# Kernel tuning notes

Measured on AMD Instinct MI355X. Metric: run time of the kernel, lower is better.

The kernel has to match this reference:

```python
import jax, jax.numpy as jnp
import numpy as np

B, C, D = 8192, 1000, 2048
CLAMP_MIN, CLAMP_MAX = 1e-12, 1e12
SEP_WEIGHT = 0.001


def setup_inputs() -> dict:
    key = jax.random.key(0)
    k1, k2, k3 = jax.random.split(key, 3)
    x = jax.random.normal(k1, (B, D), dtype=jnp.float32)
    centers = jax.random.normal(k2, (C, D), dtype=jnp.float32)
    labels = jax.random.randint(k3, (B,), 0, C, dtype=jnp.int64)
    return {"x": x, "centers": centers, "labels": labels}


def reference(x, centers, labels):
    distmat = (
        jnp.sum(x * x, axis=1, keepdims=True)
        + jnp.sum(centers * centers, axis=1)[None, :]
        - 2.0 * (x @ centers.T)
    )
    d = jnp.clip(distmat, CLAMP_MIN, CLAMP_MAX)
    mask = labels[:, None] == jnp.arange(C, dtype=labels.dtype)[None, :]  # [B, C]
    bsz = x.shape[0]
    ncls = centers.shape[0]
    # each row has exactly one True in mask -> counts are B and B*(C-1)
    center_loss = jnp.sum(jnp.where(mask, d, 0.0)) / bsz
    sep_loss = jnp.sum(jnp.where(mask, 0.0, d)) / (bsz * (ncls - 1))
    return center_loss - SEP_WEIGHT * sep_loss
```

## Files before the change

### kernel.cpp

```cpp
#include <hip/hip_runtime.h>


#define DD 2048
#define NB 8192
#define NC 1000
#define D4 (DD / 4)
#define HALF4 256
#define THREADS 256
#define XROWS 8
#define XBLOCKS ((NB / XROWS) * 2)
#define CTILES 8
#define CRG 8
#define CBLOCKS (CTILES * CRG)

#define CQ_OFF   0
#define SC_OFF   65536
#define CSQ_OFF  73728
#define PART_OFF 73984

__device__ __forceinline__ float dot4(float4 a, float4 b) {
    return a.x * b.x + a.y * b.y + a.z * b.z + a.w * b.w;
}
__device__ __forceinline__ void acc4(float4& a, float4 b) {
    a.x += b.x; a.y += b.y; a.z += b.z; a.w += b.w;
}

__global__ __launch_bounds__(THREADS) void centers_kernel(
        const float4* __restrict__ c4, float4* __restrict__ cq,
        float* __restrict__ csq_part) {
    const int t = threadIdx.x;
    const int tile = blockIdx.x & (CTILES - 1);
    const int rg = blockIdx.x >> 3;
    const int col4 = tile * 64 + (t & 63);
    const int rlane = t >> 6;
    const int row0 = rg * 125;

    float4 acc = make_float4(0.f, 0.f, 0.f, 0.f);
    float csq = 0.f;
#pragma unroll 4
    for (int r = rlane; r < 125; r += 4) {
        float4 v = c4[(size_t)(row0 + r) * D4 + col4];
        acc4(acc, v);
        csq += dot4(v, v);
    }

    __shared__ float4 lds[4][64];
    lds[rlane][t & 63] = acc;
    __syncthreads();
    if (t < 64) {
        float4 s = lds[0][t];
        acc4(s, lds[1][t]); acc4(s, lds[2][t]); acc4(s, lds[3][t]);
        cq[rg * 512 + tile * 64 + t] = s;
    }

    __shared__ float red[THREADS / 64];
    for (int off = 32; off > 0; off >>= 1) csq += __shfl_down(csq, off, 64);
    const int lane = t & 63, wv = t >> 6;
    if (lane == 0) red[wv] = csq;
    __syncthreads();
    if (t == 0)
        csq_part[blockIdx.x] = red[0] + red[1] + red[2] + red[3];
}

__global__ __launch_bounds__(THREADS) void sc_fold_kernel(
        const float4* __restrict__ cq, float4* __restrict__ sc4) {
    const int idx = blockIdx.x * THREADS + threadIdx.x;
    float4 s = cq[idx];
#pragma unroll
    for (int r = 1; r < CRG; ++r) acc4(s, cq[r * 512 + idx]);
    sc4[idx] = s;
}

__global__ __launch_bounds__(THREADS) void x_kernel(
        const float4* __restrict__ x4, const float4* __restrict__ c4,
        const int* __restrict__ labels, const float4* __restrict__ sc4,
        float4* __restrict__ partials) {
    const int t = threadIdx.x;
    const int b = blockIdx.x;
    const int rowgrp = b >> 1;
    const int h = (b & 1) * HALF4;
    const int rows0 = rowgrp * XROWS;

    const float4* xr = x4 + (size_t)rows0 * D4 + h + t;
    const float4* cbase = c4 + h + t;

    float4 xa = xr[0];
    float4 xb = xr[D4];

    const int4* l4 = (const int4*)(labels + rows0);
    const int4 la = l4[0], lb = l4[1];
    const int labs[XROWS] = {la.x, la.y, la.z, la.w, lb.x, lb.y, lb.z, lb.w};

    const float4 sc = sc4[h + t];

    float4 ca = cbase[(size_t)labs[0] * D4];
    float4 cb = cbase[(size_t)labs[1] * D4];

    float sx = 0.f, sdot = 0.f, scl = 0.f, s2 = 0.f;

#pragma unroll
    for (int r = 0; r < XROWS; ++r) {
        float4 nx, nc;
        if (r + 2 < XROWS) {
            nx = xr[(size_t)(r + 2) * D4];
            nc = cbase[(size_t)labs[r + 2] * D4];
        }
        sx   += dot4(xa, xa);
        sdot += dot4(xa, ca);
        scl  += dot4(ca, ca);
        s2   += dot4(xa, sc);
        xa = xb; ca = cb;
        if (r + 2 < XROWS) { xb = nx; cb = nc; }
    }

    __shared__ float red[4][THREADS / 64];
    for (int off = 32; off > 0; off >>= 1) {
        sx   += __shfl_down(sx, off, 64);
        sdot += __shfl_down(sdot, off, 64);
        scl  += __shfl_down(scl, off, 64);
        s2   += __shfl_down(s2, off, 64);
    }
    const int lane = t & 63, wv = t >> 6;
    if (lane == 0) {
        red[0][wv] = sx; red[1][wv] = sdot;
        red[2][wv] = scl; red[3][wv] = s2;
    }
    __syncthreads();
    if (t == 0) {
        float4 s;
        s.x = red[0][0] + red[0][1] + red[0][2] + red[0][3];
        s.y = red[1][0] + red[1][1] + red[1][2] + red[1][3];
        s.z = red[2][0] + red[2][1] + red[2][2] + red[2][3];
        s.w = red[3][0] + red[3][1] + red[3][2] + red[3][3];
        partials[b] = s;
    }
}

__global__ __launch_bounds__(THREADS) void finalize_kernel(
        const float4* __restrict__ partials, const float* __restrict__ csq_part,
        float* __restrict__ out) {
    const int t = threadIdx.x;

    double sx = 0.0, sdot = 0.0, scl = 0.0, s2 = 0.0, csq = 0.0;
    for (int i = t; i < XBLOCKS; i += THREADS) {
        float4 p = partials[i];
        sx += (double)p.x; sdot += (double)p.y;
        scl += (double)p.z; s2 += (double)p.w;
    }
    if (t < CBLOCKS) csq = (double)csq_part[t];

    __shared__ double red[5][THREADS / 64];
    for (int off = 32; off > 0; off >>= 1) {
        sx   += __shfl_down(sx, off, 64);
        sdot += __shfl_down(sdot, off, 64);
        scl  += __shfl_down(scl, off, 64);
        s2   += __shfl_down(s2, off, 64);
        csq  += __shfl_down(csq, off, 64);
    }
    const int lane = t & 63, wv = t >> 6;
    if (lane == 0) {
        red[0][wv] = sx; red[1][wv] = sdot; red[2][wv] = scl;
        red[3][wv] = s2; red[4][wv] = csq;
    }
    __syncthreads();
    if (t == 0) {
        double Sx   = red[0][0] + red[0][1] + red[0][2] + red[0][3];
        double Sdot = red[1][0] + red[1][1] + red[1][2] + red[1][3];
        double Scl  = red[2][0] + red[2][1] + red[2][2] + red[2][3];
        double S2   = red[3][0] + red[3][1] + red[3][2] + red[3][3];
        double Sc   = red[4][0] + red[4][1] + red[4][2] + red[4][3];
        double sum_all  = (double)NC * Sx + (double)NB * Sc - 2.0 * S2;
        double sum_diag = Sx + Scl - 2.0 * Sdot;
        double center_loss = sum_diag / (double)NB;
        double sep_loss =
            (sum_all - sum_diag) / ((double)NB * (double)(NC - 1));
        out[0] = (float)(center_loss - 0.001 * sep_loss);
    }
}

extern "C" void kernel_launch(void* const* d_in, const int* in_sizes, int n_in,
                              void* d_out, int out_size, void* d_ws, size_t ws_size,
                              hipStream_t stream) {
    const float4* x4 = (const float4*)d_in[0];
    const float4* c4 = (const float4*)d_in[1];
    const int* labels = (const int*)d_in[2];

    float4* cq = (float4*)((char*)d_ws + CQ_OFF);
    float4* sc = (float4*)((char*)d_ws + SC_OFF);
    float* csq_part = (float*)((char*)d_ws + CSQ_OFF);
    float4* partials = (float4*)((char*)d_ws + PART_OFF);
    float* out = (float*)d_out;

    centers_kernel<<<CBLOCKS, THREADS, 0, stream>>>(c4, cq, csq_part);
    sc_fold_kernel<<<2, THREADS, 0, stream>>>((const float4*)cq, sc);
    x_kernel<<<XBLOCKS, THREADS, 0, stream>>>(x4, c4, labels,
                                              (const float4*)sc, partials);
    finalize_kernel<<<1, THREADS, 0, stream>>>(partials, csq_part, out);
}
```

Baseline: 110.7 us.

## Counting-sort rows by label so center gathers hit cache

An extra block in the centers kernel builds a label histogram, prefix-scans it, and writes a permutation of row indices grouped by label along with the sorted labels. The x kernel then processes rows in that order, so consecutive rows share the same center row and the gathered center reads should reuse cache instead of scattering. The cost is a serial single-block sort on the critical path before x_kernel, plus x rows now read non-contiguously across a block.

```diff
diff --git a/kernel.cpp b/kernel.cpp
--- a/kernel.cpp
+++ b/kernel.cpp
@@ -17,6 +17,8 @@
 #define SC_OFF   65536
 #define CSQ_OFF  73728
 #define PART_OFF 73984
+#define PERM_OFF 106752
+#define SLAB_OFF 139520
 
 __device__ __forceinline__ float dot4(float4 a, float4 b) {
     return a.x * b.x + a.y * b.y + a.z * b.z + a.w * b.w;
@@ -26,9 +28,46 @@
 }
 
 __global__ __launch_bounds__(THREADS) void centers_kernel(
-        const float4* __restrict__ c4, float4* __restrict__ cq,
-        float* __restrict__ csq_part) {
+        const float4* __restrict__ c4, const int* __restrict__ labels,
+        float4* __restrict__ cq, float* __restrict__ csq_part,
+        int* __restrict__ perm, int* __restrict__ slab) {
     const int t = threadIdx.x;
+
+    if (blockIdx.x == CBLOCKS) {
+        __shared__ unsigned int hist[1024];
+        __shared__ unsigned int pre[1024];
+        __shared__ unsigned int off[1024];
+        for (int i = t; i < 1024; i += THREADS) hist[i] = 0u;
+        __syncthreads();
+        for (int i = t; i < NB; i += THREADS)
+            atomicAdd(&hist[labels[i]], 1u);
+        __syncthreads();
+        for (int i = t; i < 1024; i += THREADS) pre[i] = hist[i];
+        __syncthreads();
+        for (int d = 1; d < 1024; d <<= 1) {
+            unsigned int v[4];
+#pragma unroll
+            for (int k = 0; k < 4; ++k) {
+                int i = t + THREADS * k;
+                v[k] = (i >= d) ? pre[i - d] : 0u;
+            }
+            __syncthreads();
+#pragma unroll
+            for (int k = 0; k < 4; ++k) pre[t + THREADS * k] += v[k];
+            __syncthreads();
+        }
+        for (int i = t; i < 1024; i += THREADS)
+            off[i] = pre[i] - hist[i];
+        __syncthreads();
+        for (int i = t; i < NB; i += THREADS) {
+            int lb = labels[i];
+            unsigned int p = atomicAdd(&off[lb], 1u);
+            perm[p] = i;
+            slab[p] = lb;
+        }
+        return;
+    }
+
     const int tile = blockIdx.x & (CTILES - 1);
     const int rg = blockIdx.x >> 3;
     const int col4 = tile * 64 + (t & 63);
@@ -54,9 +93,9 @@
     }
 
     __shared__ float red[THREADS / 64];
-    for (int off = 32; off > 0; off >>= 1) csq += __shfl_down(csq, off, 64);
-    const int lane = t & 63, wv = t >> 6;
-    if (lane == 0) red[wv] = csq;
+    for (int offr = 32; offr > 0; offr >>= 1)
+        csq += __shfl_down(csq, offr, 64);
+    if ((t & 63) == 0) red[t >> 6] = csq;
     __syncthreads();
     if (t == 0)
         csq_part[blockIdx.x] = red[0] + red[1] + red[2] + red[3];
@@ -73,28 +112,27 @@
 
 __global__ __launch_bounds__(THREADS) void x_kernel(
         const float4* __restrict__ x4, const float4* __restrict__ c4,
-        const int* __restrict__ labels, const float4* __restrict__ sc4,
-        float4* __restrict__ partials) {
+        const int* __restrict__ perm, const int* __restrict__ slab,
+        const float4* __restrict__ sc4, float4* __restrict__ partials) {
     const int t = threadIdx.x;
     const int b = blockIdx.x;
     const int rowgrp = b >> 1;
     const int h = (b & 1) * HALF4;
-    const int rows0 = rowgrp * XROWS;
-
-    const float4* xr = x4 + (size_t)rows0 * D4 + h + t;
-    const float4* cbase = c4 + h + t;
-
-    float4 xa = xr[0];
-    float4 xb = xr[D4];
-
-    const int4* l4 = (const int4*)(labels + rows0);
-    const int4 la = l4[0], lb = l4[1];
-    const int labs[XROWS] = {la.x, la.y, la.z, la.w, lb.x, lb.y, lb.z, lb.w};
-
+    const int s0 = rowgrp * XROWS;
+
+    const int4* p4 = (const int4*)(perm + s0);
+    const int4 pa = p4[0], pb = p4[1];
+    const int rows[XROWS] = {pa.x, pa.y, pa.z, pa.w, pb.x, pb.y, pb.z, pb.w};
+    const int4* sl4 = (const int4*)(slab + s0);
+    const int4 sa = sl4[0], sb = sl4[1];
+    const int labs[XROWS] = {sa.x, sa.y, sa.z, sa.w, sb.x, sb.y, sb.z, sb.w};
+
+    const float4* xb4 = x4 + h + t;
+    const float4* cb4 = c4 + h + t;
     const float4 sc = sc4[h + t];
 
-    float4 ca = cbase[(size_t)labs[0] * D4];
-    float4 cb = cbase[(size_t)labs[1] * D4];
+    float4 xa = xb4[(size_t)rows[0] * D4], ca = cb4[(size_t)labs[0] * D4];
+    float4 xb = xb4[(size_t)rows[1] * D4], cb = cb4[(size_t)labs[1] * D4];
 
     float sx = 0.f, sdot = 0.f, scl = 0.f, s2 = 0.f;
 
@@ -102,8 +140,8 @@
     for (int r = 0; r < XROWS; ++r) {
         float4 nx, nc;
         if (r + 2 < XROWS) {
-            nx = xr[(size_t)(r + 2) * D4];
-            nc = cbase[(size_t)labs[r + 2] * D4];
+            nx = xb4[(size_t)rows[r + 2] * D4];
+            nc = cb4[(size_t)labs[r + 2] * D4];
         }
         sx   += dot4(xa, xa);
         sdot += dot4(xa, ca);
@@ -189,11 +227,14 @@
     float4* sc = (float4*)((char*)d_ws + SC_OFF);
     float* csq_part = (float*)((char*)d_ws + CSQ_OFF);
     float4* partials = (float4*)((char*)d_ws + PART_OFF);
+    int* perm = (int*)((char*)d_ws + PERM_OFF);
+    int* slab = (int*)((char*)d_ws + SLAB_OFF);
     float* out = (float*)d_out;
 
-    centers_kernel<<<CBLOCKS, THREADS, 0, stream>>>(c4, cq, csq_part);
+    centers_kernel<<<CBLOCKS + 1, THREADS, 0, stream>>>(c4, labels, cq,
+                                                        csq_part, perm, slab);
     sc_fold_kernel<<<2, THREADS, 0, stream>>>((const float4*)cq, sc);
-    x_kernel<<<XBLOCKS, THREADS, 0, stream>>>(x4, c4, labels,
+    x_kernel<<<XBLOCKS, THREADS, 0, stream>>>(x4, c4, perm, slab,
                                               (const float4*)sc, partials);
     finalize_kernel<<<1, THREADS, 0, stream>>>(partials, csq_part, out);
 }
```

New measurement: 127.5 us. +15.1%, slower.
